# Kernel tuning notes

Measured on AMD Instinct MI355X. Metric: run time of the kernel, lower is better.

Reference implementation:

```python
import jax, jax.numpy as jnp
import numpy as np

B, N, DIM = 16, 1024, 512
H, DH = 8, 64  # heads, dim_head; inner_dim = H*DH = 512
MASK_VAL = -1e-9  # value ASSIGNED (not added) to diagonal, per original code


def setup_inputs() -> dict:
    key = jax.random.key(0)
    ks = jax.random.split(key, 8)
    w = 0.02  # small init so softmax is not saturated
    x = jax.random.normal(ks[0], (B, N, DIM), dtype=jnp.float32)
    Wq = jax.random.normal(ks[1], (DIM, H * DH), dtype=jnp.float32) * w
    Wkv = jax.random.normal(ks[2], (DIM, 2 * H * DH), dtype=jnp.float32) * w
    scale = jnp.full((H,), DH ** -0.5, dtype=jnp.float32)  # nn.Parameter(scale*ones(heads))
    mix_pre = jax.random.normal(ks[3], (H, H), dtype=jnp.float32) * w
    mix_post = jax.random.normal(ks[4], (H, H), dtype=jnp.float32) * w
    Wout = jax.random.normal(ks[5], (H * DH, DIM), dtype=jnp.float32) * w
    bout = jnp.zeros((DIM,), dtype=jnp.float32)
    return {"x": x, "Wq": Wq, "Wkv": Wkv, "scale": scale,
            "mix_pre": mix_pre, "mix_post": mix_post, "Wout": Wout, "bout": bout}


def reference(x, Wq, Wkv, scale, mix_pre, mix_post, Wout, bout):
    b, n, _ = x.shape
    # projections -> [b, h, n, d]
    q = (x @ Wq).reshape(b, n, H, DH).transpose(0, 2, 1, 3)
    kv = (x @ Wkv).reshape(b, n, 2, H, DH)
    k = kv[:, :, 0].transpose(0, 2, 1, 3)
    v = kv[:, :, 1].transpose(0, 2, 1, 3)
    # LMSA: per-head learned scale
    dots = jnp.einsum('bhid,bhjd->bhij', q, k) * scale[None, :, None, None]
    # if_patch_attn: set diagonal entries to -1e-9 (assignment, as in torch)
    eye = jnp.eye(n, dtype=bool)
    dots = jnp.where(eye, jnp.float32(MASK_VAL), dots)
    # talking heads: pre-softmax head mix
    dots = jnp.einsum('bhij,hg->bgij', dots, mix_pre)
    attn = jax.nn.softmax(dots, axis=-1)
    # post-softmax head mix
    attn = jnp.einsum('bhij,hg->bgij', attn, mix_post)
    out = jnp.einsum('bhij,bhjd->bhid', attn, v)  # [b,h,n,d]
    out = out.transpose(0, 2, 1, 3).reshape(b, n, H * DH)
    return out @ Wout + bout
```

## Files before the change

kernel.cpp:

```cpp
#include <hip/hip_runtime.h>
#include <math.h>


typedef short bf16x8 __attribute__((ext_vector_type(8)));
typedef float f32x4 __attribute__((ext_vector_type(4)));

__device__ __forceinline__ f32x4 mfma16(bf16x8 a, bf16x8 b, f32x4 c) {
  return __builtin_amdgcn_mfma_f32_16x16x32_bf16(a, b, c, 0, 0, 0);
}

__device__ __forceinline__ unsigned short f2bf(float f) {
  unsigned u = __float_as_uint(f);
  u = (u + 0x7fffu + ((u >> 16) & 1u)) >> 16;
  return (unsigned short)u;
}

__device__ __forceinline__ void splitbf(float f, unsigned short& hi,
                                        unsigned short& lo) {
  hi = f2bf(f);
  float fh = __uint_as_float((unsigned)hi << 16);
  lo = f2bf(f - fh);
}

__device__ __forceinline__ f32x4 zero4() {
  f32x4 z = {0.f, 0.f, 0.f, 0.f};
  return z;
}

namespace {

constexpr int kB = 16, kN = 1024, kH = 8;

__global__ __launch_bounds__(256) void prep(
    const float* __restrict__ Wq, const float* __restrict__ Wkv,
    const float* __restrict__ Wout, unsigned short* __restrict__ WTh,
    unsigned short* __restrict__ WTl, unsigned short* __restrict__ WoTh,
    unsigned short* __restrict__ WoTl) {
  int id = blockIdx.x * 256 + threadIdx.x;
  unsigned short h, l;
  if (id < 1536 * 512) {
    int n = id >> 9, k = id & 511;
    float v = (n < 512) ? Wq[(size_t)k * 512 + n]
                        : Wkv[(size_t)k * 1024 + (n - 512)];
    splitbf(v, h, l);
    WTh[id] = h; WTl[id] = l;
  } else {
    int id2 = id - 1536 * 512;
    int n = id2 >> 9, k = id2 & 511;
    splitbf(Wout[(size_t)k * 512 + n], h, l);
    WoTh[id2] = h; WoTl[id2] = l;
  }
}

__global__ __launch_bounds__(256) void gemm_qkv(
    const float* __restrict__ X, const unsigned short* __restrict__ WTh,
    const unsigned short* __restrict__ WTl, const float* __restrict__ scale,
    unsigned short* __restrict__ Qh, unsigned short* __restrict__ Ql,
    unsigned short* __restrict__ Kh, unsigned short* __restrict__ Kl,
    unsigned short* __restrict__ Vh, unsigned short* __restrict__ Vl) {
  __shared__ unsigned short Ah[128 * 72], Al[128 * 72];
  __shared__ unsigned short Bh[128 * 72], Bl[128 * 72];
  const int tid = threadIdx.x;
  const int n0 = blockIdx.x * 128, m0 = blockIdx.y * 128;
  const int w = tid >> 6, lane = tid & 63, quad = lane >> 4, ln = lane & 15;
  const int mw = (w >> 1) * 64, nw = (w & 1) * 64;
  const int srow = tid >> 3, schk = (tid & 7) * 8;
  f32x4 acc[4][4];
#pragma unroll
  for (int i = 0; i < 4; ++i)
#pragma unroll
    for (int j = 0; j < 4; ++j) acc[i][j] = zero4();
  for (int k0 = 0; k0 < 512; k0 += 64) {
    float xa[4][8];
    uint4 bh4[4], bl4[4];
#pragma unroll
    for (int c2 = 0; c2 < 4; ++c2) {
      const float* xs = X + (size_t)(m0 + c2 * 32 + srow) * 512 + k0 + schk;
      *(float4*)&xa[c2][0] = *(const float4*)xs;
      *(float4*)&xa[c2][4] = *(const float4*)(xs + 4);
      size_t boff = (size_t)(n0 + c2 * 32 + srow) * 512 + k0 + schk;
      bh4[c2] = *(const uint4*)(WTh + boff);
      bl4[c2] = *(const uint4*)(WTl + boff);
    }
    __syncthreads();
#pragma unroll
    for (int c2 = 0; c2 < 4; ++c2) {
      unsigned short hh[8], ll[8];
#pragma unroll
      for (int e = 0; e < 8; ++e) splitbf(xa[c2][e], hh[e], ll[e]);
      uint4 ph, pl;
      ph.x = hh[0] | ((unsigned)hh[1] << 16); pl.x = ll[0] | ((unsigned)ll[1] << 16);
      ph.y = hh[2] | ((unsigned)hh[3] << 16); pl.y = ll[2] | ((unsigned)ll[3] << 16);
      ph.z = hh[4] | ((unsigned)hh[5] << 16); pl.z = ll[4] | ((unsigned)ll[5] << 16);
      ph.w = hh[6] | ((unsigned)hh[7] << 16); pl.w = ll[6] | ((unsigned)ll[7] << 16);
      *(uint4*)&Ah[(c2 * 32 + srow) * 72 + schk] = ph;
      *(uint4*)&Al[(c2 * 32 + srow) * 72 + schk] = pl;
      *(uint4*)&Bh[(c2 * 32 + srow) * 72 + schk] = bh4[c2];
      *(uint4*)&Bl[(c2 * 32 + srow) * 72 + schk] = bl4[c2];
    }
    __syncthreads();
#pragma unroll
    for (int ks = 0; ks < 2; ++ks) {
      bf16x8 afh[4], afl[4], bfh[4], bfl[4];
#pragma unroll
      for (int t = 0; t < 4; ++t) {
        int ao = (mw + t * 16 + ln) * 72 + ks * 32 + quad * 8;
        int bo = (nw + t * 16 + ln) * 72 + ks * 32 + quad * 8;
        afh[t] = *(const bf16x8*)&Ah[ao];
        afl[t] = *(const bf16x8*)&Al[ao];
        bfh[t] = *(const bf16x8*)&Bh[bo];
        bfl[t] = *(const bf16x8*)&Bl[bo];
      }
#pragma unroll
      for (int mt = 0; mt < 4; ++mt)
#pragma unroll
        for (int nt = 0; nt < 4; ++nt) {
          acc[mt][nt] = mfma16(afh[mt], bfh[nt], acc[mt][nt]);
          acc[mt][nt] = mfma16(afh[mt], bfl[nt], acc[mt][nt]);
          acc[mt][nt] = mfma16(afl[mt], bfh[nt], acc[mt][nt]);
        }
    }
  }
  const int region = n0 >> 9;
#pragma unroll
  for (int nt = 0; nt < 4; ++nt) {
    const int col = n0 + nw + nt * 16 + ln;
    const int local = col - region * 512;
    const int hh = local >> 6, d = local & 63;
    const float sc = (region == 0) ? scale[hh] : 1.f;
#pragma unroll
    for (int mt = 0; mt < 4; ++mt) {
#pragma unroll
      for (int r = 0; r < 4; ++r) {
        const int row = m0 + mw + mt * 16 + quad * 4 + r;
        const int b = row >> 10, i = row & 1023;
        unsigned short vh, vl;
        splitbf(acc[mt][nt][r] * sc, vh, vl);
        if (region == 0) {
          size_t o = (((size_t)(b * 8 + hh) * 1024 + i) << 6) + d;
          Qh[o] = vh; Ql[o] = vl;
        } else if (region == 1) {
          size_t o = (((size_t)(b * 8 + hh) * 1024 + i) << 6) + d;
          Kh[o] = vh; Kl[o] = vl;
        } else {
          size_t o = (((size_t)(b * 8 + hh) * 64 + d) << 10) + i;
          Vh[o] = vh; Vl[o] = vl;
        }
      }
    }
  }
}

__global__ __launch_bounds__(128) void attn_fused(
    const unsigned short* __restrict__ Qh_g, const unsigned short* __restrict__ Ql_g,
    const unsigned short* __restrict__ Kh, const unsigned short* __restrict__ Kl,
    const unsigned short* __restrict__ Vh, const unsigned short* __restrict__ Vl,
    const float* __restrict__ mix_pre, const float* __restrict__ mix_post,
    float* __restrict__ OA) {
  __shared__ unsigned short Qsh[128 * 72];
  __shared__ unsigned short Wsh[128 * 40], Wsl[128 * 40];
  __shared__ float mixp_s[64], mixq_s[64], dfix_s[8];
  __shared__ float Ils[8][16];
  float* lred = (float*)Wsh;
  const int tid = threadIdx.x;
  const int b = blockIdx.y, i0 = blockIdx.x * 16;
  const int w = tid >> 6, lane = tid & 63, quad = lane >> 4, ln = lane & 15;
  const int jh = w * 16;
  if (tid < 64) { mixp_s[tid] = mix_pre[tid]; mixq_s[tid] = mix_post[tid]; }
  if (tid < 8) {
    float s = 0.f;
#pragma unroll
    for (int h = 0; h < 8; ++h) s += mix_pre[h * 8 + tid];
    dfix_s[tid] = -1e-9f * s;
  }
#pragma unroll
  for (int c = 0; c < 8; ++c) {
    int v = tid + 128 * c;
    int row = v >> 3, chk = (v & 7) * 8;
    int h = row >> 4, ii = row & 15;
    *(uint4*)&Qsh[row * 72 + chk] =
        *(const uint4*)(Qh_g + (((size_t)(b * 8 + h) * 1024 + i0 + ii) << 6) + chk);
  }
  bf16x8 qlo[8][2];
#pragma unroll
  for (int h = 0; h < 8; ++h)
#pragma unroll
    for (int ks = 0; ks < 2; ++ks)
      qlo[h][ks] = *(const bf16x8*)(
          Ql_g + (((size_t)(b * 8 + h) * 1024 + i0 + ln) << 6) + ks * 32 + quad * 8);
  __syncthreads();
  const int ig0 = i0 + quad * 4;

  float l[8][4];
#pragma unroll
  for (int a = 0; a < 8; ++a)
#pragma unroll
    for (int r = 0; r < 4; ++r) l[a][r] = 0.f;
  for (int j0 = 0; j0 < 1024; j0 += 32) {
    bf16x8 kh_r[2][2], kl_r[2][2];
#pragma unroll
    for (int ks = 0; ks < 2; ++ks) {
      size_t kro = (((size_t)(b * 8 + 0) * 1024 + j0 + jh + ln) << 6) + ks * 32 + quad * 8;
      kh_r[0][ks] = *(const bf16x8*)(Kh + kro);
      kl_r[0][ks] = *(const bf16x8*)(Kl + kro);
    }
    f32x4 S[8];
    int cur = 0;
#pragma unroll
    for (int h = 0; h < 8; ++h) {
      const int nxt = cur ^ 1;
      if (h < 7) {
#pragma unroll
        for (int ks = 0; ks < 2; ++ks) {
          size_t kro = (((size_t)(b * 8 + h + 1) * 1024 + j0 + jh + ln) << 6) + ks * 32 + quad * 8;
          kh_r[nxt][ks] = *(const bf16x8*)(Kh + kro);
          kl_r[nxt][ks] = *(const bf16x8*)(Kl + kro);
        }
      }
      f32x4 acc = zero4();
#pragma unroll
      for (int ks = 0; ks < 2; ++ks) {
        bf16x8 ah = *(const bf16x8*)&Qsh[(h * 16 + ln) * 72 + ks * 32 + quad * 8];
        acc = mfma16(ah, kh_r[cur][ks], acc);
        acc = mfma16(ah, kl_r[cur][ks], acc);
        acc = mfma16(qlo[h][ks], kh_r[cur][ks], acc);
      }
      S[h] = acc;
      cur = nxt;
    }
    const int dr = (j0 + jh + ln) - ig0;
#pragma unroll
    for (int a = 0; a < 8; ++a) {
      f32x4 sm = S[0] * mixp_s[a];
#pragma unroll
      for (int h = 1; h < 8; ++h) sm += S[h] * mixp_s[h * 8 + a];
      const float df = dfix_s[a];
#pragma unroll
      for (int r = 0; r < 4; ++r) {
        float v = (r == dr) ? df : sm[r];
        l[a][r] += __expf(v);
      }
    }
  }
#pragma unroll
  for (int off = 1; off < 16; off <<= 1)
#pragma unroll
    for (int a = 0; a < 8; ++a)
#pragma unroll
      for (int r = 0; r < 4; ++r) l[a][r] += __shfl_xor(l[a][r], off);
  if (ln == 0) {
#pragma unroll
    for (int a = 0; a < 8; ++a)
#pragma unroll
      for (int r = 0; r < 4; ++r) lred[(w * 8 + a) * 16 + quad * 4 + r] = l[a][r];
  }
  __syncthreads();
  {
    int a = tid >> 4, i = tid & 15;
    Ils[a][i] = 1.f / (lred[a * 16 + i] + lred[(8 + a) * 16 + i]);
  }
  __syncthreads();

  f32x4 O[4][4];
#pragma unroll
  for (int cc = 0; cc < 4; ++cc)
#pragma unroll
    for (int nt = 0; nt < 4; ++nt) O[cc][nt] = zero4();
  for (int j0 = 0; j0 < 1024; j0 += 32) {
    bf16x8 kh_r[2][2], kl_r[2][2];
#pragma unroll
    for (int ks = 0; ks < 2; ++ks) {
      size_t kro = (((size_t)(b * 8 + 0) * 1024 + j0 + jh + ln) << 6) + ks * 32 + quad * 8;
      kh_r[0][ks] = *(const bf16x8*)(Kh + kro);
      kl_r[0][ks] = *(const bf16x8*)(Kl + kro);
    }
    f32x4 S[8];
    int cur = 0;
#pragma unroll
    for (int h = 0; h < 8; ++h) {
      const int nxt = cur ^ 1;
      if (h < 7) {
#pragma unroll
        for (int ks = 0; ks < 2; ++ks) {
          size_t kro = (((size_t)(b * 8 + h + 1) * 1024 + j0 + jh + ln) << 6) + ks * 32 + quad * 8;
          kh_r[nxt][ks] = *(const bf16x8*)(Kh + kro);
          kl_r[nxt][ks] = *(const bf16x8*)(Kl + kro);
        }
      }
      f32x4 acc = zero4();
#pragma unroll
      for (int ks = 0; ks < 2; ++ks) {
        bf16x8 ah = *(const bf16x8*)&Qsh[(h * 16 + ln) * 72 + ks * 32 + quad * 8];
        acc = mfma16(ah, kh_r[cur][ks], acc);
        acc = mfma16(ah, kl_r[cur][ks], acc);
        acc = mfma16(qlo[h][ks], kh_r[cur][ks], acc);
      }
      S[h] = acc;
      cur = nxt;
    }
    const int dr = (j0 + jh + ln) - ig0;
    f32x4 P[8];
#pragma unroll
    for (int a = 0; a < 8; ++a) {
      f32x4 sm = S[0] * mixp_s[a];
#pragma unroll
      for (int h = 1; h < 8; ++h) sm += S[h] * mixp_s[h * 8 + a];
      const float df = dfix_s[a];
      f32x4 il4 = *(const f32x4*)&Ils[a][quad * 4];
      f32x4 p;
#pragma unroll
      for (int r = 0; r < 4; ++r) {
        float v = (r == dr) ? df : sm[r];
        p[r] = __expf(v) * il4[r];
      }
      P[a] = p;
    }
#pragma unroll
    for (int c = 0; c < 8; ++c) {
      f32x4 wv = P[0] * mixq_s[c];
#pragma unroll
      for (int a = 1; a < 8; ++a) wv += P[a] * mixq_s[a * 8 + c];
#pragma unroll
      for (int r = 0; r < 4; ++r) {
        unsigned short vh, vl;
        splitbf(wv[r], vh, vl);
        int o = (c * 16 + quad * 4 + r) * 40 + jh + ln;
        Wsh[o] = vh; Wsl[o] = vl;
      }
    }
    bf16x8 vbh[2][4], vbl[2][4];
    {
      const int c = w * 4;
#pragma unroll
      for (int nt = 0; nt < 4; ++nt) {
        size_t vo = (((size_t)(b * 8 + c) * 64 + nt * 16 + ln) << 10) + j0 + quad * 8;
        vbh[0][nt] = *(const bf16x8*)(Vh + vo);
        vbl[0][nt] = *(const bf16x8*)(Vl + vo);
      }
    }
    __syncthreads();
    int vcur = 0;
#pragma unroll
    for (int cc = 0; cc < 4; ++cc) {
      const int c = w * 4 + cc;
      const int vnxt = vcur ^ 1;
      if (cc < 3) {
#pragma unroll
        for (int nt = 0; nt < 4; ++nt) {
          size_t vo = (((size_t)(b * 8 + c + 1) * 64 + nt * 16 + ln) << 10) + j0 + quad * 8;
          vbh[vnxt][nt] = *(const bf16x8*)(Vh + vo);
          vbl[vnxt][nt] = *(const bf16x8*)(Vl + vo);
        }
      }
      bf16x8 a_h = *(const bf16x8*)&Wsh[(c * 16 + ln) * 40 + quad * 8];
      bf16x8 a_l = *(const bf16x8*)&Wsl[(c * 16 + ln) * 40 + quad * 8];
#pragma unroll
      for (int nt = 0; nt < 4; ++nt) {
        O[cc][nt] = mfma16(a_h, vbh[vcur][nt], O[cc][nt]);
        O[cc][nt] = mfma16(a_h, vbl[vcur][nt], O[cc][nt]);
        O[cc][nt] = mfma16(a_l, vbh[vcur][nt], O[cc][nt]);
      }
      vcur = vnxt;
    }
    __syncthreads();
  }
#pragma unroll
  for (int cc = 0; cc < 4; ++cc)
#pragma unroll
    for (int nt = 0; nt < 4; ++nt)
#pragma unroll
      for (int r = 0; r < 4; ++r) {
        const int i = i0 + quad * 4 + r;
        const int col = (w * 4 + cc) * 64 + nt * 16 + ln;
        OA[((size_t)(b * 1024 + i) << 9) + col] = O[cc][nt][r];
      }
}

__global__ __launch_bounds__(256) void gemm_out(
    const float* __restrict__ A, const unsigned short* __restrict__ BTh,
    const unsigned short* __restrict__ BTl, const float* __restrict__ bias,
    float* __restrict__ Out) {
  __shared__ unsigned short Ah[128 * 72], Al[128 * 72];
  __shared__ unsigned short Bh[128 * 72], Bl[128 * 72];
  const int tid = threadIdx.x;
  const int n0 = blockIdx.x * 128, m0 = blockIdx.y * 128;
  const int w = tid >> 6, lane = tid & 63, quad = lane >> 4, ln = lane & 15;
  const int mw = (w >> 1) * 64, nw = (w & 1) * 64;
  const int srow = tid >> 3, schk = (tid & 7) * 8;
  f32x4 acc[4][4];
#pragma unroll
  for (int i = 0; i < 4; ++i)
#pragma unroll
    for (int j = 0; j < 4; ++j) acc[i][j] = zero4();
  for (int k0 = 0; k0 < 512; k0 += 64) {
    float xa[4][8];
    uint4 bh4[4], bl4[4];
#pragma unroll
    for (int c2 = 0; c2 < 4; ++c2) {
      const float* xs = A + (size_t)(m0 + c2 * 32 + srow) * 512 + k0 + schk;
      *(float4*)&xa[c2][0] = *(const float4*)xs;
      *(float4*)&xa[c2][4] = *(const float4*)(xs + 4);
      size_t boff = (size_t)(n0 + c2 * 32 + srow) * 512 + k0 + schk;
      bh4[c2] = *(const uint4*)(BTh + boff);
      bl4[c2] = *(const uint4*)(BTl + boff);
    }
    __syncthreads();
#pragma unroll
    for (int c2 = 0; c2 < 4; ++c2) {
      unsigned short hh[8], ll[8];
#pragma unroll
      for (int e = 0; e < 8; ++e) splitbf(xa[c2][e], hh[e], ll[e]);
      uint4 ph, pl;
      ph.x = hh[0] | ((unsigned)hh[1] << 16); pl.x = ll[0] | ((unsigned)ll[1] << 16);
      ph.y = hh[2] | ((unsigned)hh[3] << 16); pl.y = ll[2] | ((unsigned)ll[3] << 16);
      ph.z = hh[4] | ((unsigned)hh[5] << 16); pl.z = ll[4] | ((unsigned)ll[5] << 16);
      ph.w = hh[6] | ((unsigned)hh[7] << 16); pl.w = ll[6] | ((unsigned)ll[7] << 16);
      *(uint4*)&Ah[(c2 * 32 + srow) * 72 + schk] = ph;
      *(uint4*)&Al[(c2 * 32 + srow) * 72 + schk] = pl;
      *(uint4*)&Bh[(c2 * 32 + srow) * 72 + schk] = bh4[c2];
      *(uint4*)&Bl[(c2 * 32 + srow) * 72 + schk] = bl4[c2];
    }
    __syncthreads();
#pragma unroll
    for (int ks = 0; ks < 2; ++ks) {
      bf16x8 afh[4], afl[4], bfh[4], bfl[4];
#pragma unroll
      for (int t = 0; t < 4; ++t) {
        int ao = (mw + t * 16 + ln) * 72 + ks * 32 + quad * 8;
        int bo = (nw + t * 16 + ln) * 72 + ks * 32 + quad * 8;
        afh[t] = *(const bf16x8*)&Ah[ao];
        afl[t] = *(const bf16x8*)&Al[ao];
        bfh[t] = *(const bf16x8*)&Bh[bo];
        bfl[t] = *(const bf16x8*)&Bl[bo];
      }
#pragma unroll
      for (int mt = 0; mt < 4; ++mt)
#pragma unroll
        for (int nt = 0; nt < 4; ++nt) {
          acc[mt][nt] = mfma16(afh[mt], bfh[nt], acc[mt][nt]);
          acc[mt][nt] = mfma16(afh[mt], bfl[nt], acc[mt][nt]);
          acc[mt][nt] = mfma16(afl[mt], bfh[nt], acc[mt][nt]);
        }
    }
  }
#pragma unroll
  for (int nt = 0; nt < 4; ++nt) {
    const int col = n0 + nw + nt * 16 + ln;
    const float bcol = bias[col];
#pragma unroll
    for (int mt = 0; mt < 4; ++mt) {
#pragma unroll
      for (int r = 0; r < 4; ++r) {
        const int row = m0 + mw + mt * 16 + quad * 4 + r;
        Out[(size_t)row * 512 + col] = acc[mt][nt][r] + bcol;
      }
    }
  }
}

}

extern "C" void kernel_launch(void* const* d_in, const int* in_sizes, int n_in,
                              void* d_out, int out_size, void* d_ws, size_t ws_size,
                              hipStream_t stream) {
  const float* x        = (const float*)d_in[0];
  const float* Wq       = (const float*)d_in[1];
  const float* Wkv      = (const float*)d_in[2];
  const float* scale    = (const float*)d_in[3];
  const float* mix_pre  = (const float*)d_in[4];
  const float* mix_post = (const float*)d_in[5];
  const float* Wout     = (const float*)d_in[6];
  const float* bout     = (const float*)d_in[7];
  float* out = (float*)d_out;

  char* p = (char*)d_ws;
  const size_t qsz = (size_t)kB * kH * kN * 64;
  unsigned short* WTh  = (unsigned short*)p; p += (size_t)1536 * 512 * 2;
  unsigned short* WTl  = (unsigned short*)p; p += (size_t)1536 * 512 * 2;
  unsigned short* WoTh = (unsigned short*)p; p += (size_t)512 * 512 * 2;
  unsigned short* WoTl = (unsigned short*)p; p += (size_t)512 * 512 * 2;
  unsigned short* Qh   = (unsigned short*)p; p += qsz * 2;
  unsigned short* Ql   = (unsigned short*)p; p += qsz * 2;
  unsigned short* Kh   = (unsigned short*)p; p += qsz * 2;
  unsigned short* Kl   = (unsigned short*)p; p += qsz * 2;
  unsigned short* Vh   = (unsigned short*)p; p += qsz * 2;
  unsigned short* Vl   = (unsigned short*)p; p += qsz * 2;
  float* OA = (float*)p; p += (size_t)kB * kN * 512 * 4;

  prep<<<4096, 256, 0, stream>>>(Wq, Wkv, Wout, WTh, WTl, WoTh, WoTl);
  gemm_qkv<<<dim3(12, 128), 256, 0, stream>>>(x, WTh, WTl, scale,
                                              Qh, Ql, Kh, Kl, Vh, Vl);
  attn_fused<<<dim3(64, 16), 128, 0, stream>>>(Qh, Ql, Kh, Kl, Vh, Vl,
                                               mix_pre, mix_post, OA);
  gemm_out<<<dim3(4, 128), 256, 0, stream>>>(OA, WoTh, WoTl, bout, out);
}
```

Before: 1.442 ms.

## Split attention into score and PV kernels, storing exp scores in workspace

The fused attention kernel ran the QK^T and talking-heads pre-mix twice, once for the softmax denominator and once for the output. It is now split into attn_score, which computes exp scores once, writes them to a float workspace and stores inverse row sums, and attn_pv, which reloads them, normalises, applies the post-mix and multiplies by V. Both use 256-thread blocks and launches are chunked over batch and row blocks to fit the available workspace. This removes the duplicated QK^T MFMA work but adds a large round trip of exp scores through global memory (about 512 KB per block of 16 rows), and possibly many kernel launches if the workspace is small.

```diff
diff --git a/kernel.cpp b/kernel.cpp
--- a/kernel.cpp
+++ b/kernel.cpp
@@ -151,22 +151,19 @@
   }
 }
 
-__global__ __launch_bounds__(128) void attn_fused(
+__global__ __launch_bounds__(256) void attn_score(
     const unsigned short* __restrict__ Qh_g, const unsigned short* __restrict__ Ql_g,
     const unsigned short* __restrict__ Kh, const unsigned short* __restrict__ Kl,
-    const unsigned short* __restrict__ Vh, const unsigned short* __restrict__ Vl,
-    const float* __restrict__ mix_pre, const float* __restrict__ mix_post,
-    float* __restrict__ OA) {
+    const float* __restrict__ mix_pre, float* __restrict__ Pp,
+    float* __restrict__ IL, int b0, int ib0) {
   __shared__ unsigned short Qsh[128 * 72];
-  __shared__ unsigned short Wsh[128 * 40], Wsl[128 * 40];
-  __shared__ float mixp_s[64], mixq_s[64], dfix_s[8];
-  __shared__ float Ils[8][16];
-  float* lred = (float*)Wsh;
+  __shared__ float mixp_s[64], dfix_s[8];
+  __shared__ float lred[512];
   const int tid = threadIdx.x;
-  const int b = blockIdx.y, i0 = blockIdx.x * 16;
+  const int b = b0 + blockIdx.y, ib = ib0 + blockIdx.x, i0 = ib * 16;
   const int w = tid >> 6, lane = tid & 63, quad = lane >> 4, ln = lane & 15;
   const int jh = w * 16;
-  if (tid < 64) { mixp_s[tid] = mix_pre[tid]; mixq_s[tid] = mix_post[tid]; }
+  if (tid < 64) mixp_s[tid] = mix_pre[tid];
   if (tid < 8) {
     float s = 0.f;
 #pragma unroll
@@ -174,35 +171,32 @@
     dfix_s[tid] = -1e-9f * s;
   }
 #pragma unroll
-  for (int c = 0; c < 8; ++c) {
-    int v = tid + 128 * c;
+  for (int c = 0; c < 4; ++c) {
+    int v = tid + 256 * c;
     int row = v >> 3, chk = (v & 7) * 8;
     int h = row >> 4, ii = row & 15;
     *(uint4*)&Qsh[row * 72 + chk] =
         *(const uint4*)(Qh_g + (((size_t)(b * 8 + h) * 1024 + i0 + ii) << 6) + chk);
   }
-  bf16x8 qlo[8][2];
-#pragma unroll
-  for (int h = 0; h < 8; ++h)
-#pragma unroll
-    for (int ks = 0; ks < 2; ++ks)
-      qlo[h][ks] = *(const bf16x8*)(
-          Ql_g + (((size_t)(b * 8 + h) * 1024 + i0 + ln) << 6) + ks * 32 + quad * 8);
   __syncthreads();
   const int ig0 = i0 + quad * 4;
-
   float l[8][4];
 #pragma unroll
   for (int a = 0; a < 8; ++a)
 #pragma unroll
     for (int r = 0; r < 4; ++r) l[a][r] = 0.f;
-  for (int j0 = 0; j0 < 1024; j0 += 32) {
-    bf16x8 kh_r[2][2], kl_r[2][2];
+  float* Pblk = Pp + ((size_t)(blockIdx.y * gridDim.x + blockIdx.x) << 17);
+  const size_t qoff = (((size_t)(b * 8) * 1024 + i0 + ln) << 6) + quad * 8;
+#pragma unroll 1
+  for (int j0 = 0; j0 < 1024; j0 += 64) {
+    const int jj = j0 + jh + ln;
+    bf16x8 kh_r[2][2], kl_r[2][2], ql_r[2][2];
 #pragma unroll
     for (int ks = 0; ks < 2; ++ks) {
-      size_t kro = (((size_t)(b * 8 + 0) * 1024 + j0 + jh + ln) << 6) + ks * 32 + quad * 8;
+      size_t kro = (((size_t)(b * 8) * 1024 + jj) << 6) + ks * 32 + quad * 8;
       kh_r[0][ks] = *(const bf16x8*)(Kh + kro);
       kl_r[0][ks] = *(const bf16x8*)(Kl + kro);
+      ql_r[0][ks] = *(const bf16x8*)(Ql_g + qoff + ks * 32);
     }
     f32x4 S[8];
     int cur = 0;
@@ -212,9 +206,10 @@
       if (h < 7) {
 #pragma unroll
         for (int ks = 0; ks < 2; ++ks) {
-          size_t kro = (((size_t)(b * 8 + h + 1) * 1024 + j0 + jh + ln) << 6) + ks * 32 + quad * 8;
+          size_t kro = (((size_t)(b * 8 + h + 1) * 1024 + jj) << 6) + ks * 32 + quad * 8;
           kh_r[nxt][ks] = *(const bf16x8*)(Kh + kro);
           kl_r[nxt][ks] = *(const bf16x8*)(Kl + kro);
+          ql_r[nxt][ks] = *(const bf16x8*)(Ql_g + qoff + (size_t)(h + 1) * 65536 + ks * 32);
         }
       }
       f32x4 acc = zero4();
@@ -223,23 +218,27 @@
         bf16x8 ah = *(const bf16x8*)&Qsh[(h * 16 + ln) * 72 + ks * 32 + quad * 8];
         acc = mfma16(ah, kh_r[cur][ks], acc);
         acc = mfma16(ah, kl_r[cur][ks], acc);
-        acc = mfma16(qlo[h][ks], kh_r[cur][ks], acc);
+        acc = mfma16(ql_r[cur][ks], kh_r[cur][ks], acc);
       }
       S[h] = acc;
       cur = nxt;
     }
-    const int dr = (j0 + jh + ln) - ig0;
+    const int dr = jj - ig0;
+    float* pj = Pblk + (size_t)jj * 16 + quad * 4;
 #pragma unroll
     for (int a = 0; a < 8; ++a) {
       f32x4 sm = S[0] * mixp_s[a];
 #pragma unroll
       for (int h = 1; h < 8; ++h) sm += S[h] * mixp_s[h * 8 + a];
       const float df = dfix_s[a];
+      f32x4 pv;
 #pragma unroll
       for (int r = 0; r < 4; ++r) {
-        float v = (r == dr) ? df : sm[r];
-        l[a][r] += __expf(v);
-      }
+        float vv = (r == dr) ? df : sm[r];
+        pv[r] = __expf(vv);
+        l[a][r] += pv[r];
+      }
+      *(f32x4*)(pj + (a << 14)) = pv;
     }
   }
 #pragma unroll
@@ -252,126 +251,128 @@
 #pragma unroll
     for (int a = 0; a < 8; ++a)
 #pragma unroll
-      for (int r = 0; r < 4; ++r) lred[(w * 8 + a) * 16 + quad * 4 + r] = l[a][r];
+      for (int r = 0; r < 4; ++r)
+        lred[(w * 8 + a) * 16 + quad * 4 + r] = l[a][r];
   }
   __syncthreads();
+  if (tid < 128) {
+    int a = tid >> 4, i = tid & 15;
+    float s = lred[a * 16 + i] + lred[(8 + a) * 16 + i] +
+              lred[(16 + a) * 16 + i] + lred[(24 + a) * 16 + i];
+    IL[(((size_t)b * 8 + a) << 10) + i0 + i] = 1.f / s;
+  }
+}
+
+__global__ __launch_bounds__(256) void attn_pv(
+    const float* __restrict__ Pp, const float* __restrict__ IL,
+    const unsigned short* __restrict__ Vh, const unsigned short* __restrict__ Vl,
+    const float* __restrict__ mix_post, float* __restrict__ OA,
+    int b0, int ib0) {
+  __shared__ unsigned short Wsh[128 * 72], Wsl[128 * 72];
+  __shared__ float mixq_s[64];
+  __shared__ float Ils[8][16];
+  const int tid = threadIdx.x;
+  const int b = b0 + blockIdx.y, ib = ib0 + blockIdx.x, i0 = ib * 16;
+  const int w = tid >> 6, lane = tid & 63, quad = lane >> 4, ln = lane & 15;
+  const int jh = w * 16;
+  if (tid < 64) mixq_s[tid] = mix_post[tid];
+  if (tid < 128) {
+    int a = tid >> 4, i = tid & 15;
+    Ils[a][i] = IL[(((size_t)b * 8 + a) << 10) + i0 + i];
+  }
+  __syncthreads();
+  const float* Pblk = Pp + ((size_t)(blockIdx.y * gridDim.x + blockIdx.x) << 17);
+  const int cw = w * 2;
+  f32x4 O[2][4];
+#pragma unroll
+  for (int cc = 0; cc < 2; ++cc)
+#pragma unroll
+    for (int nt = 0; nt < 4; ++nt) O[cc][nt] = zero4();
+  f32x4 praw[8];
   {
-    int a = tid >> 4, i = tid & 15;
-    Ils[a][i] = 1.f / (lred[a * 16 + i] + lred[(8 + a) * 16 + i]);
-  }
-  __syncthreads();
-
-  f32x4 O[4][4];
-#pragma unroll
-  for (int cc = 0; cc < 4; ++cc)
-#pragma unroll
-    for (int nt = 0; nt < 4; ++nt) O[cc][nt] = zero4();
-  for (int j0 = 0; j0 < 1024; j0 += 32) {
-    bf16x8 kh_r[2][2], kl_r[2][2];
-#pragma unroll
-    for (int ks = 0; ks < 2; ++ks) {
-      size_t kro = (((size_t)(b * 8 + 0) * 1024 + j0 + jh + ln) << 6) + ks * 32 + quad * 8;
-      kh_r[0][ks] = *(const bf16x8*)(Kh + kro);
-      kl_r[0][ks] = *(const bf16x8*)(Kl + kro);
-    }
-    f32x4 S[8];
-    int cur = 0;
-#pragma unroll
-    for (int h = 0; h < 8; ++h) {
-      const int nxt = cur ^ 1;
-      if (h < 7) {
-#pragma unroll
-        for (int ks = 0; ks < 2; ++ks) {
-          size_t kro = (((size_t)(b * 8 + h + 1) * 1024 + j0 + jh + ln) << 6) + ks * 32 + quad * 8;
-          kh_r[nxt][ks] = *(const bf16x8*)(Kh + kro);
-          kl_r[nxt][ks] = *(const bf16x8*)(Kl + kro);
-        }
-      }
-      f32x4 acc = zero4();
-#pragma unroll
-      for (int ks = 0; ks < 2; ++ks) {
-        bf16x8 ah = *(const bf16x8*)&Qsh[(h * 16 + ln) * 72 + ks * 32 + quad * 8];
-        acc = mfma16(ah, kh_r[cur][ks], acc);
-        acc = mfma16(ah, kl_r[cur][ks], acc);
-        acc = mfma16(qlo[h][ks], kh_r[cur][ks], acc);
-      }
-      S[h] = acc;
-      cur = nxt;
-    }
-    const int dr = (j0 + jh + ln) - ig0;
-    f32x4 P[8];
-#pragma unroll
-    for (int a = 0; a < 8; ++a) {
-      f32x4 sm = S[0] * mixp_s[a];
-#pragma unroll
-      for (int h = 1; h < 8; ++h) sm += S[h] * mixp_s[h * 8 + a];
-      const float df = dfix_s[a];
-      f32x4 il4 = *(const f32x4*)&Ils[a][quad * 4];
-      f32x4 p;
+    const float* pj = Pblk + (size_t)(jh + ln) * 16 + quad * 4;
+#pragma unroll
+    for (int a = 0; a < 8; ++a) praw[a] = *(const f32x4*)(pj + (a << 14));
+  }
+  f32x4 pa[8];
+#pragma unroll
+  for (int a = 0; a < 8; ++a) pa[a] = praw[a] * *(const f32x4*)&Ils[a][quad * 4];
+  bf16x8 vbh[2][4], vbl[2][4];
+#pragma unroll
+  for (int nt = 0; nt < 4; ++nt) {
+    size_t vo = (((size_t)(b * 8 + cw) * 64 + nt * 16 + ln) << 10) + quad * 8;
+    vbh[0][nt] = *(const bf16x8*)(Vh + vo);
+    vbl[0][nt] = *(const bf16x8*)(Vl + vo);
+  }
+#pragma unroll 1
+  for (int t = 0; t < 16; ++t) {
+    const int j0 = t * 64;
+#pragma unroll
+    for (int c = 0; c < 8; ++c) {
+      f32x4 wv = pa[0] * mixq_s[c];
+#pragma unroll
+      for (int a = 1; a < 8; ++a) wv += pa[a] * mixq_s[a * 8 + c];
 #pragma unroll
       for (int r = 0; r < 4; ++r) {
-        float v = (r == dr) ? df : sm[r];
-        p[r] = __expf(v) * il4[r];
-      }
-      P[a] = p;
-    }
-#pragma unroll
-    for (int c = 0; c < 8; ++c) {
-      f32x4 wv = P[0] * mixq_s[c];
-#pragma unroll
-      for (int a = 1; a < 8; ++a) wv += P[a] * mixq_s[a * 8 + c];
-#pragma unroll
-      for (int r = 0; r < 4; ++r) {
-        unsigned short vh, vl;
-        splitbf(wv[r], vh, vl);
-        int o = (c * 16 + quad * 4 + r) * 40 + jh + ln;
-        Wsh[o] = vh; Wsl[o] = vl;
-      }
-    }
-    bf16x8 vbh[2][4], vbl[2][4];
-    {
-      const int c = w * 4;
-#pragma unroll
-      for (int nt = 0; nt < 4; ++nt) {
-        size_t vo = (((size_t)(b * 8 + c) * 64 + nt * 16 + ln) << 10) + j0 + quad * 8;
-        vbh[0][nt] = *(const bf16x8*)(Vh + vo);
-        vbl[0][nt] = *(const bf16x8*)(Vl + vo);
+        unsigned short vhh, vll;
+        splitbf(wv[r], vhh, vll);
+        int o = (c * 16 + quad * 4 + r) * 72 + jh + ln;
+        Wsh[o] = vhh; Wsl[o] = vll;
       }
     }
     __syncthreads();
-    int vcur = 0;
-#pragma unroll
-    for (int cc = 0; cc < 4; ++cc) {
-      const int c = w * 4 + cc;
-      const int vnxt = vcur ^ 1;
-      if (cc < 3) {
+#pragma unroll
+    for (int s = 0; s < 4; ++s) {
+      const int cc = s >> 1, ks = s & 1;
+      const int c = cw + cc;
+      const int vcur = s & 1, vnxt = vcur ^ 1;
+      if (s < 3) {
+        const int cc2 = (s + 1) >> 1, ks2 = (s + 1) & 1;
 #pragma unroll
         for (int nt = 0; nt < 4; ++nt) {
-          size_t vo = (((size_t)(b * 8 + c + 1) * 64 + nt * 16 + ln) << 10) + j0 + quad * 8;
+          size_t vo = (((size_t)(b * 8 + cw + cc2) * 64 + nt * 16 + ln) << 10) +
+                      j0 + ks2 * 32 + quad * 8;
           vbh[vnxt][nt] = *(const bf16x8*)(Vh + vo);
           vbl[vnxt][nt] = *(const bf16x8*)(Vl + vo);
         }
-      }
-      bf16x8 a_h = *(const bf16x8*)&Wsh[(c * 16 + ln) * 40 + quad * 8];
-      bf16x8 a_l = *(const bf16x8*)&Wsl[(c * 16 + ln) * 40 + quad * 8];
+      } else if (t < 15) {
+#pragma unroll
+        for (int nt = 0; nt < 4; ++nt) {
+          size_t vo = (((size_t)(b * 8 + cw) * 64 + nt * 16 + ln) << 10) +
+                      j0 + 64 + quad * 8;
+          vbh[vnxt][nt] = *(const bf16x8*)(Vh + vo);
+          vbl[vnxt][nt] = *(const bf16x8*)(Vl + vo);
+        }
+      }
+      if (s == 0 && t < 15) {
+        const float* pj = Pblk + (size_t)(j0 + 64 + jh + ln) * 16 + quad * 4;
+#pragma unroll
+        for (int a = 0; a < 8; ++a) praw[a] = *(const f32x4*)(pj + (a << 14));
+      }
+      bf16x8 a_h = *(const bf16x8*)&Wsh[(c * 16 + ln) * 72 + ks * 32 + quad * 8];
+      bf16x8 a_l = *(const bf16x8*)&Wsl[(c * 16 + ln) * 72 + ks * 32 + quad * 8];
 #pragma unroll
       for (int nt = 0; nt < 4; ++nt) {
         O[cc][nt] = mfma16(a_h, vbh[vcur][nt], O[cc][nt]);
         O[cc][nt] = mfma16(a_h, vbl[vcur][nt], O[cc][nt]);
         O[cc][nt] = mfma16(a_l, vbh[vcur][nt], O[cc][nt]);
       }
-      vcur = vnxt;
     }
     __syncthreads();
-  }
-#pragma unroll
-  for (int cc = 0; cc < 4; ++cc)
+    if (t < 15) {
+#pragma unroll
+      for (int a = 0; a < 8; ++a)
+        pa[a] = praw[a] * *(const f32x4*)&Ils[a][quad * 4];
+    }
+  }
+#pragma unroll
+  for (int cc = 0; cc < 2; ++cc)
 #pragma unroll
     for (int nt = 0; nt < 4; ++nt)
 #pragma unroll
       for (int r = 0; r < 4; ++r) {
         const int i = i0 + quad * 4 + r;
-        const int col = (w * 4 + cc) * 64 + nt * 16 + ln;
+        const int col = (cw + cc) * 64 + nt * 16 + ln;
         OA[((size_t)(b * 1024 + i) << 9) + col] = O[cc][nt][r];
       }
 }
@@ -486,11 +487,37 @@
   unsigned short* Vh   = (unsigned short*)p; p += qsz * 2;
   unsigned short* Vl   = (unsigned short*)p; p += qsz * 2;
   float* OA = (float*)p; p += (size_t)kB * kN * 512 * 4;
+  float* ILp = (float*)p; p += (size_t)131072 * 4;
+  float* Pp = (float*)p;
+
+  const size_t fixed = (size_t)(p - (char*)d_ws);
+  const size_t avail = (ws_size > fixed) ? (ws_size - fixed) : 0;
+  const size_t per_ib = (size_t)131072 * 4;
+  const size_t per_b = per_ib * 64;
+  int cb, cib;
+  if (avail >= per_b) {
+    cb = (int)(avail / per_b);
+    if (cb > 16) cb = 16;
+    cib = 64;
+  } else {
+    cb = 1;
+    cib = (int)(avail / per_ib);
+    if (cib > 64) cib = 64;
+    if (cib < 1) cib = 1;
+  }
 
   prep<<<4096, 256, 0, stream>>>(Wq, Wkv, Wout, WTh, WTl, WoTh, WoTl);
   gemm_qkv<<<dim3(12, 128), 256, 0, stream>>>(x, WTh, WTl, scale,
                                               Qh, Ql, Kh, Kl, Vh, Vl);
-  attn_fused<<<dim3(64, 16), 128, 0, stream>>>(Qh, Ql, Kh, Kl, Vh, Vl,
-                                               mix_pre, mix_post, OA);
+  for (int b0 = 0; b0 < 16; b0 += cb) {
+    const int nb = (b0 + cb <= 16) ? cb : (16 - b0);
+    for (int ib0 = 0; ib0 < 64; ib0 += cib) {
+      const int nib = (ib0 + cib <= 64) ? cib : (64 - ib0);
+      attn_score<<<dim3(nib, nb), 256, 0, stream>>>(Qh, Ql, Kh, Kl, mix_pre,
+                                                    Pp, ILp, b0, ib0);
+      attn_pv<<<dim3(nib, nb), 256, 0, stream>>>(Pp, ILp, Vh, Vl, mix_post,
+                                                 OA, b0, ib0);
+    }
+  }
   gemm_out<<<dim3(4, 128), 256, 0, stream>>>(OA, WoTh, WoTl, bout, out);
 }
```

After: 1.913 ms. 32.7% more time.
